# Performance work log

Hardware: AMD Instinct MI355X
Metric: run time of the kernel (lower is better)

Reference implementation:

```python
import jax, jax.numpy as jnp
import numpy as np

B, S, DIM = 4, 2048, 64
NUM_CODES = 65536
KCODES = 8


def setup_inputs() -> dict:
    key = jax.random.key(0)
    k1, k2 = jax.random.split(key)
    x = jax.random.normal(k1, (B, S, DIM), dtype=jnp.float32)
    codebook = jax.random.normal(k2, (NUM_CODES, DIM), dtype=jnp.float32)
    return {"x": x, "codebook": codebook}


def reference(x, codebook):
    """EuclideanSnapFunction.forward, keep_k_codes path with no disabled codes.

    logits = -cdist(x, codebook, p=2); topk(kcodes); embedding gather; mean.
    sqrt is monotonic, so top-k on negative *squared* distance yields identical
    indices (and identical outputs) while avoiding the sqrt.
    """
    x2 = jnp.sum(x * x, axis=-1, keepdims=True)          # [B,S,1]
    c2 = jnp.sum(codebook * codebook, axis=-1)           # [N]
    xc = jnp.einsum("bsd,nd->bsn", x, codebook)          # [B,S,N]
    neg_d2 = 2.0 * xc - x2 - c2                           # = -squared dist
    _, codebook_ids = jax.lax.top_k(neg_d2, KCODES)      # [B,S,K]
    codes = codebook[codebook_ids]                        # [B,S,K,D] gather
    outputs = codes.sum(axis=-2) / KCODES                 # [B,S,D]
    return outputs, codebook_ids
```

## Files before the change

### kernel.cpp

```cpp
#include <hip/hip_runtime.h>
#include <float.h>

#define DIM     64
#define NCODES  65536
#define KC      8
#define NQ      8192
#define KROW    80
#define CS      32
#define CHUNK   (NCODES/CS)
#define NITER   (CHUNK/32)
#define NVIEW   64
#define CAP     12
#define DELTA   1.5f
#define MAXSUR  384

typedef __bf16 bf16x8 __attribute__((ext_vector_type(8)));
typedef float  f32x16 __attribute__((ext_vector_type(16)));
typedef unsigned short u16x8 __attribute__((ext_vector_type(8)));

static __device__ __forceinline__ unsigned short f2bf(float f) {
    unsigned u = __float_as_uint(f);
    u += 0x7FFFu + ((u >> 16) & 1u);
    return (unsigned short)(u >> 16);
}

#define RJ(j) (((j) & 3) + 8 * ((j) >> 2))

__global__ __launch_bounds__(256) void k_conv_cb(const float* __restrict__ cb,
                                                 unsigned short* __restrict__ cbb) {
    int n = blockIdx.x * 256 + threadIdx.x;
    const float4* src = (const float4*)(cb + (size_t)n * DIM);
    unsigned short* dst = cbb + (size_t)n * KROW;
    float s = 0.f;
#pragma unroll
    for (int c = 0; c < 8; ++c) {
        float4 f0 = src[2 * c], f1 = src[2 * c + 1];
        s = fmaf(f0.x, f0.x, s); s = fmaf(f0.y, f0.y, s);
        s = fmaf(f0.z, f0.z, s); s = fmaf(f0.w, f0.w, s);
        s = fmaf(f1.x, f1.x, s); s = fmaf(f1.y, f1.y, s);
        s = fmaf(f1.z, f1.z, s); s = fmaf(f1.w, f1.w, s);
        u16x8 o;
        o[0] = f2bf(2.f * f0.x); o[1] = f2bf(2.f * f0.y);
        o[2] = f2bf(2.f * f0.z); o[3] = f2bf(2.f * f0.w);
        o[4] = f2bf(2.f * f1.x); o[5] = f2bf(2.f * f1.y);
        o[6] = f2bf(2.f * f1.z); o[7] = f2bf(2.f * f1.w);
        *(u16x8*)(dst + c * 8) = o;
    }
    unsigned short hi = f2bf(s);
    float hif = __uint_as_float(((unsigned)hi) << 16);
    unsigned short lo = f2bf(s - hif);
    u16x8 p = { (unsigned short)(hi ^ 0x8000u), (unsigned short)(lo ^ 0x8000u),
                0, 0, 0, 0, 0, 0 };
    *(u16x8*)(dst + 64) = p;
    u16x8 z = {0, 0, 0, 0, 0, 0, 0, 0};
    *(u16x8*)(dst + 72) = z;
}

__global__ __launch_bounds__(256) void k_conv_x(const float* __restrict__ x,
                                                unsigned short* __restrict__ xb) {
    int n = blockIdx.x * 256 + threadIdx.x;
    const float4* src = (const float4*)(x + (size_t)n * DIM);
    unsigned short* dst = xb + (size_t)n * KROW;
#pragma unroll
    for (int c = 0; c < 8; ++c) {
        float4 f0 = src[2 * c], f1 = src[2 * c + 1];
        u16x8 o;
        o[0] = f2bf(f0.x); o[1] = f2bf(f0.y); o[2] = f2bf(f0.z); o[3] = f2bf(f0.w);
        o[4] = f2bf(f1.x); o[5] = f2bf(f1.y); o[6] = f2bf(f1.z); o[7] = f2bf(f1.w);
        *(u16x8*)(dst + c * 8) = o;
    }
    u16x8 p = {0x3F80u, 0x3F80u, 0, 0, 0, 0, 0, 0};
    *(u16x8*)(dst + 64) = p;
    u16x8 z = {0, 0, 0, 0, 0, 0, 0, 0};
    *(u16x8*)(dst + 72) = z;
}

__device__ __forceinline__ float tmax16(const f32x16& a) {
    const float m0 = fmaxf(fmaxf(a[0],  a[1]),  a[2]);
    const float m1 = fmaxf(fmaxf(a[3],  a[4]),  a[5]);
    const float m2 = fmaxf(fmaxf(a[6],  a[7]),  a[8]);
    const float m3 = fmaxf(fmaxf(a[9],  a[10]), a[11]);
    const float m4 = fmaxf(fmaxf(a[12], a[13]), a[14]);
    const float n0 = fmaxf(fmaxf(m0, m1), m2);
    const float n1 = fmaxf(fmaxf(m3, m4), a[15]);
    return fmaxf(n0, n1);
}

__global__ __launch_bounds__(256, 4) void k_scanA(const unsigned short* __restrict__ cbb_,
                                                  const unsigned short* __restrict__ xb_,
                                                  float* __restrict__ top1) {
    const __bf16* cbv = (const __bf16*)cbb_;
    const __bf16* xbv = (const __bf16*)xb_;
    const int tid = threadIdx.x, lane = tid & 63, wv = tid >> 6;
    const int laneh = lane >> 5;
    const int qg = blockIdx.x >> 5;
    const int cs = blockIdx.x & 31;
    const int qA = qg * 256 + wv * 64 + (lane & 31);
    const int qB = qA + 32;
    const int cbase = cs * CHUNK;
    const int view = cs * 2 + laneh;

    bf16x8 bfrA[5], bfrB[5];
    {
        const __bf16* bp = xbv + (size_t)qA * KROW + laneh * 8;
#pragma unroll
        for (int s = 0; s < 5; ++s) bfrA[s] = *(const bf16x8*)(bp + s * 16);
        bp += (size_t)32 * KROW;
#pragma unroll
        for (int s = 0; s < 5; ++s) bfrB[s] = *(const bf16x8*)(bp + s * 16);
    }

    float t1a = -FLT_MAX, t1b = -FLT_MAX;

    const __bf16* ap = cbv + (size_t)(cbase + (lane & 31)) * KROW + laneh * 8;
    bf16x8 fA[5], fB[5];
#pragma unroll
    for (int s = 0; s < 5; ++s) fA[s] = *(const bf16x8*)(ap + s * 16);
#pragma unroll
    for (int s = 0; s < 5; ++s) fB[s] = *(const bf16x8*)(ap + 32 * KROW + s * 16);
    ap += 64 * KROW;

    for (int it = 0; it < NITER; it += 2) {
        {
            f32x16 acc = {0,0,0,0, 0,0,0,0, 0,0,0,0, 0,0,0,0};
#pragma unroll
            for (int s = 0; s < 5; ++s)
                acc = __builtin_amdgcn_mfma_f32_32x32x16_bf16(fA[s], bfrA[s], acc, 0, 0, 0);
            t1a = fmaxf(t1a, tmax16(acc));
            f32x16 acc2 = {0,0,0,0, 0,0,0,0, 0,0,0,0, 0,0,0,0};
#pragma unroll
            for (int s = 0; s < 5; ++s)
                acc2 = __builtin_amdgcn_mfma_f32_32x32x16_bf16(fA[s], bfrB[s], acc2, 0, 0, 0);
#pragma unroll
            for (int s = 0; s < 5; ++s) fA[s] = *(const bf16x8*)(ap + s * 16);
            t1b = fmaxf(t1b, tmax16(acc2));
        }
        {
            f32x16 acc = {0,0,0,0, 0,0,0,0, 0,0,0,0, 0,0,0,0};
#pragma unroll
            for (int s = 0; s < 5; ++s)
                acc = __builtin_amdgcn_mfma_f32_32x32x16_bf16(fB[s], bfrA[s], acc, 0, 0, 0);
            t1a = fmaxf(t1a, tmax16(acc));
            f32x16 acc2 = {0,0,0,0, 0,0,0,0, 0,0,0,0, 0,0,0,0};
#pragma unroll
            for (int s = 0; s < 5; ++s)
                acc2 = __builtin_amdgcn_mfma_f32_32x32x16_bf16(fB[s], bfrB[s], acc2, 0, 0, 0);
#pragma unroll
            for (int s = 0; s < 5; ++s) fB[s] = *(const bf16x8*)(ap + 32 * KROW + s * 16);
            t1b = fmaxf(t1b, tmax16(acc2));
        }
        ap += 64 * KROW;
    }

    top1[(size_t)qA * NVIEW + view] = t1a;
    top1[(size_t)qB * NVIEW + view] = t1b;
}

__global__ __launch_bounds__(256) void k_thresh(const float* __restrict__ top1,
                                                float* __restrict__ thrm) {
    const int lane = threadIdx.x & 63;
    const int q = blockIdx.x * 4 + (threadIdx.x >> 6);
    float v = top1[(size_t)q * NVIEW + lane];
    float mx = -FLT_MAX;
#pragma unroll
    for (int r = 0; r < 8; ++r) {
        mx = v;
#pragma unroll
        for (int off = 32; off; off >>= 1) mx = fmaxf(mx, __shfl_xor(mx, off, 64));
        if (v == mx) v = -FLT_MAX;
    }
    if (lane == 0) thrm[q] = mx - DELTA;
}

__global__ __launch_bounds__(256, 4) void k_collect(const unsigned short* __restrict__ cbb_,
                                                    const unsigned short* __restrict__ xb_,
                                                    const float* __restrict__ thrm,
                                                    unsigned short* __restrict__ cand,
                                                    unsigned short* __restrict__ cnt) {
    const __bf16* cbv = (const __bf16*)cbb_;
    const __bf16* xbv = (const __bf16*)xb_;
    const int tid = threadIdx.x, lane = tid & 63, wv = tid >> 6;
    const int laneh = lane >> 5;
    const int qg = blockIdx.x >> 5;
    const int cs = blockIdx.x & 31;
    const int qA = qg * 256 + wv * 64 + (lane & 31);
    const int qB = qA + 32;
    const int cbase = cs * CHUNK;
    const int view = cs * 2 + laneh;

    bf16x8 bfrA[5], bfrB[5];
    {
        const __bf16* bp = xbv + (size_t)qA * KROW + laneh * 8;
#pragma unroll
        for (int s = 0; s < 5; ++s) bfrA[s] = *(const bf16x8*)(bp + s * 16);
        bp += (size_t)32 * KROW;
#pragma unroll
        for (int s = 0; s < 5; ++s) bfrB[s] = *(const bf16x8*)(bp + s * 16);
    }
    const float TmA = thrm[qA];
    const float TmB = thrm[qB];
    unsigned cA = 0, cB = 0;
    unsigned short* bufA = cand + ((size_t)qA * NVIEW + view) * CAP;
    unsigned short* bufB = cand + ((size_t)qB * NVIEW + view) * CAP;

    const __bf16* ap = cbv + (size_t)(cbase + (lane & 31)) * KROW + laneh * 8;
    bf16x8 fA[5], fB[5];
#pragma unroll
    for (int s = 0; s < 5; ++s) fA[s] = *(const bf16x8*)(ap + s * 16);
#pragma unroll
    for (int s = 0; s < 5; ++s) fB[s] = *(const bf16x8*)(ap + 32 * KROW + s * 16);
    ap += 64 * KROW;

    for (int it = 0; it < NITER; it += 2) {
        {
            const int code0 = cbase + it * 32 + 4 * laneh;
            f32x16 acc = {0,0,0,0, 0,0,0,0, 0,0,0,0, 0,0,0,0};
#pragma unroll
            for (int s = 0; s < 5; ++s)
                acc = __builtin_amdgcn_mfma_f32_32x32x16_bf16(fA[s], bfrA[s], acc, 0, 0, 0);
            if (__any(tmax16(acc) >= TmA)) {
#pragma unroll
                for (int j = 0; j < 16; ++j)
                    if (acc[j] >= TmA) { if (cA < CAP) bufA[cA] = (unsigned short)(code0 + RJ(j)); ++cA; }
            }
            f32x16 acc2 = {0,0,0,0, 0,0,0,0, 0,0,0,0, 0,0,0,0};
#pragma unroll
            for (int s = 0; s < 5; ++s)
                acc2 = __builtin_amdgcn_mfma_f32_32x32x16_bf16(fA[s], bfrB[s], acc2, 0, 0, 0);
#pragma unroll
            for (int s = 0; s < 5; ++s) fA[s] = *(const bf16x8*)(ap + s * 16);
            if (__any(tmax16(acc2) >= TmB)) {
#pragma unroll
                for (int j = 0; j < 16; ++j)
                    if (acc2[j] >= TmB) { if (cB < CAP) bufB[cB] = (unsigned short)(code0 + RJ(j)); ++cB; }
            }
        }
        {
            const int code0 = cbase + (it + 1) * 32 + 4 * laneh;
            f32x16 acc = {0,0,0,0, 0,0,0,0, 0,0,0,0, 0,0,0,0};
#pragma unroll
            for (int s = 0; s < 5; ++s)
                acc = __builtin_amdgcn_mfma_f32_32x32x16_bf16(fB[s], bfrA[s], acc, 0, 0, 0);
            if (__any(tmax16(acc) >= TmA)) {
#pragma unroll
                for (int j = 0; j < 16; ++j)
                    if (acc[j] >= TmA) { if (cA < CAP) bufA[cA] = (unsigned short)(code0 + RJ(j)); ++cA; }
            }
            f32x16 acc2 = {0,0,0,0, 0,0,0,0, 0,0,0,0, 0,0,0,0};
#pragma unroll
            for (int s = 0; s < 5; ++s)
                acc2 = __builtin_amdgcn_mfma_f32_32x32x16_bf16(fB[s], bfrB[s], acc2, 0, 0, 0);
#pragma unroll
            for (int s = 0; s < 5; ++s) fB[s] = *(const bf16x8*)(ap + 32 * KROW + s * 16);
            if (__any(tmax16(acc2) >= TmB)) {
#pragma unroll
                for (int j = 0; j < 16; ++j)
                    if (acc2[j] >= TmB) { if (cB < CAP) bufB[cB] = (unsigned short)(code0 + RJ(j)); ++cB; }
            }
        }
        ap += 64 * KROW;
    }
    cnt[(size_t)qA * NVIEW + view] = (unsigned short)(cA < CAP ? cA : CAP);
    cnt[(size_t)qB * NVIEW + view] = (unsigned short)(cB < CAP ? cB : CAP);
}

__device__ __forceinline__ float np_pairwise_sq64(const float* __restrict__ p) {
    float r[8];
#pragma unroll
    for (int j = 0; j < 8; ++j) r[j] = __fmul_rn(p[j], p[j]);
#pragma unroll
    for (int k = 1; k < 8; ++k)
#pragma unroll
        for (int j = 0; j < 8; ++j)
            r[j] = __fadd_rn(r[j], __fmul_rn(p[8 * k + j], p[8 * k + j]));
    const float t01 = __fadd_rn(r[0], r[1]);
    const float t23 = __fadd_rn(r[2], r[3]);
    const float t45 = __fadd_rn(r[4], r[5]);
    const float t67 = __fadd_rn(r[6], r[7]);
    return __fadd_rn(__fadd_rn(t01, t23), __fadd_rn(t45, t67));
}

__device__ __forceinline__ float score_key(const float* __restrict__ xr,
                                           const float* __restrict__ cr,
                                           float x2e) {
    float xc = 0.f;
#pragma unroll
    for (int d = 0; d < DIM; ++d) xc = __builtin_fmaf(cr[d], xr[d], xc);
    const float c2e = np_pairwise_sq64(cr);
    return __fsub_rn(__fsub_rn(__fmul_rn(2.0f, xc), x2e), c2e);
}

__global__ __launch_bounds__(256) void k_rescore(const float* __restrict__ x,
                                                 const float* __restrict__ cb,
                                                 const unsigned short* __restrict__ cand,
                                                 const unsigned short* __restrict__ cnt,
                                                 float* __restrict__ out0,
                                                 float* __restrict__ out1) {
    __shared__ int s_ids[4][MAXSUR];
    const int lane = threadIdx.x & 63;
    const int wvi = threadIdx.x >> 6;
    const int q = blockIdx.x * 4 + wvi;
    const float* xr = x + ((size_t)q << 6);
    const float x2e = np_pairwise_sq64(xr);

    const int c = cnt[(size_t)q * NVIEW + lane];
    int p = c;
#pragma unroll
    for (int off = 1; off < 64; off <<= 1) {
        const int t = __shfl_up(p, off, 64);
        if (lane >= off) p += t;
    }
    const int excl = p - c;
    int total = __shfl(p, 63, 64);
    if (total > MAXSUR) total = MAXSUR;
    const unsigned short* src = cand + ((size_t)q * NVIEW + lane) * CAP;
    for (int k = 0; k < c; ++k) {
        const int dst = excl + k;
        if (dst < MAXSUR) s_ids[wvi][dst] = src[k];
    }
    __syncthreads();

    float vv[6]; int id[6];
#pragma unroll
    for (int s = 0; s < 6; ++s) {
        vv[s] = -FLT_MAX; id[s] = 1 << 20;
        if (s * 64 < total) {
            const int pos = lane + 64 * s;
            if (pos < total) {
                const int idv = s_ids[wvi][pos];
                id[s] = idv;
                vv[s] = score_key(xr, cb + (size_t)idv * DIM, x2e);
            }
        }
    }

    double accd = 0.0;
#pragma unroll
    for (int rep = 0; rep < KC; ++rep) {
        float bv = vv[0]; int bi = id[0];
#pragma unroll
        for (int s = 1; s < 6; ++s)
            if (vv[s] > bv || (vv[s] == bv && id[s] < bi)) { bv = vv[s]; bi = id[s]; }
#pragma unroll
        for (int off = 32; off; off >>= 1) {
            const float ov = __shfl_xor(bv, off, 64);
            const int   oi = __shfl_xor(bi, off, 64);
            if (ov > bv || (ov == bv && oi < bi)) { bv = ov; bi = oi; }
        }
        if (lane == 0) out1[q * KC + rep] = (float)bi;
        accd += (double)cb[(size_t)bi * DIM + lane];
#pragma unroll
        for (int s = 0; s < 6; ++s) if (id[s] == bi) vv[s] = -FLT_MAX;
    }
    out0[(size_t)q * DIM + lane] = (float)(accd * 0.125);
}

extern "C" void kernel_launch(void* const* d_in, const int* in_sizes, int n_in,
                              void* d_out, int out_size, void* d_ws, size_t ws_size,
                              hipStream_t stream) {
    const float* x  = (const float*)d_in[0];
    const float* cb = (const float*)d_in[1];

    char* ws = (char*)d_ws;
    unsigned short* cbb  = (unsigned short*)ws;
    unsigned short* xb   = (unsigned short*)(ws + (size_t)NCODES * KROW * 2);
    float*          top1 = (float*)(ws + (size_t)NCODES * KROW * 2
                                       + (size_t)NQ * KROW * 2);
    float*          thrm = (float*)((char*)top1 + (size_t)NQ * NVIEW * 4);
    unsigned short* cnt  = (unsigned short*)((char*)thrm + (size_t)NQ * 4);
    unsigned short* cand = (unsigned short*)((char*)cnt + (size_t)NQ * NVIEW * 2);

    float* out0 = (float*)d_out;
    float* out1 = (float*)d_out + (size_t)NQ * DIM;

    k_conv_cb<<<NCODES / 256, 256, 0, stream>>>(cb, cbb);
    k_conv_x <<<NQ / 256,     256, 0, stream>>>(x, xb);
    k_scanA  <<<1024,         256, 0, stream>>>(cbb, xb, top1);
    k_thresh <<<NQ / 4,       256, 0, stream>>>(top1, thrm);
    k_collect<<<1024,         256, 0, stream>>>(cbb, xb, thrm, cand, cnt);
    k_rescore<<<NQ / 4,       256, 0, stream>>>(x, cb, cand, cnt, out0, out1);
}
```

Baseline: 218.1 us.

## Stage codebook tiles through double-buffered LDS and split codebook into 64 chunks

The scan and collect kernels now cooperatively load 64-code codebook tiles into double-buffered shared memory and read MFMA operands from LDS, instead of each wave loading its own copy straight from global memory. Four waves in a block share one tile, which cuts redundant global and L2 traffic. The codebook split also goes from 32 to 64 chunks, so the grid doubles to 2048 blocks and there are 128 views per query with a per-view cap of 6. This adds a block barrier every iteration and changes the threshold and rescore indexing. Halving the per-view cap raises the risk of candidate truncation.

Result: slower. 224.8 us (+3.1%).

```diff
diff --git a/kernel.cpp b/kernel.cpp
--- a/kernel.cpp
+++ b/kernel.cpp
@@ -6,11 +6,15 @@
 #define KC      8
 #define NQ      8192
 #define KROW    80
-#define CS      32
+#define GPITCH  160
+#define LPITCH  176
+#define TILEG   5120
+#define TILEL   5632
+#define CS      64
 #define CHUNK   (NCODES/CS)
 #define NITER   (CHUNK/32)
-#define NVIEW   64
-#define CAP     12
+#define NVIEW   128
+#define CAP     6
 #define DELTA   1.5f
 #define MAXSUR  384
 
@@ -86,19 +90,31 @@
     return fmaxf(n0, n1);
 }
 
+__device__ __forceinline__ float4 stage_ld(const char* gt, int t, int r, int h) {
+    const int tile = (t >= 5) ? 1 : 0;
+    const int g16 = (h + 2 * (t - tile * 5)) * 16;
+    return *(const float4*)(gt + tile * TILEG + r * GPITCH + g16);
+}
+__device__ __forceinline__ void stage_st(unsigned char* lb, int t, int r, int h, float4 v) {
+    const int tile = (t >= 5) ? 1 : 0;
+    const int g16 = (h + 2 * (t - tile * 5)) * 16;
+    *(float4*)(lb + tile * TILEL + r * LPITCH + g16) = v;
+}
+
 __global__ __launch_bounds__(256, 4) void k_scanA(const unsigned short* __restrict__ cbb_,
                                                   const unsigned short* __restrict__ xb_,
                                                   float* __restrict__ top1) {
-    const __bf16* cbv = (const __bf16*)cbb_;
+    __shared__ __align__(16) unsigned char smem[2][2 * TILEL];
     const __bf16* xbv = (const __bf16*)xb_;
     const int tid = threadIdx.x, lane = tid & 63, wv = tid >> 6;
-    const int laneh = lane >> 5;
-    const int qg = blockIdx.x >> 5;
-    const int cs = blockIdx.x & 31;
-    const int qA = qg * 256 + wv * 64 + (lane & 31);
+    const int laneh = lane >> 5, lrow = lane & 31;
+    const int qg = blockIdx.x >> 6;
+    const int cs = blockIdx.x & 63;
+    const int qA = qg * 256 + wv * 64 + lrow;
     const int qB = qA + 32;
     const int cbase = cs * CHUNK;
     const int view = cs * 2 + laneh;
+    const char* cbbytes = (const char*)cbb_;
 
     bf16x8 bfrA[5], bfrB[5];
     {
@@ -110,46 +126,47 @@
         for (int s = 0; s < 5; ++s) bfrB[s] = *(const bf16x8*)(bp + s * 16);
     }
 
+    {
+        const char* gt = cbbytes + (size_t)cbase * GPITCH;
+        stage_st(smem[0], wv,     lrow, laneh, stage_ld(gt, wv,     lrow, laneh));
+        stage_st(smem[0], wv + 4, lrow, laneh, stage_ld(gt, wv + 4, lrow, laneh));
+        if (wv < 2)
+            stage_st(smem[0], wv + 8, lrow, laneh, stage_ld(gt, wv + 8, lrow, laneh));
+    }
+    __syncthreads();
+
     float t1a = -FLT_MAX, t1b = -FLT_MAX;
-
-    const __bf16* ap = cbv + (size_t)(cbase + (lane & 31)) * KROW + laneh * 8;
-    bf16x8 fA[5], fB[5];
-#pragma unroll
-    for (int s = 0; s < 5; ++s) fA[s] = *(const bf16x8*)(ap + s * 16);
-#pragma unroll
-    for (int s = 0; s < 5; ++s) fB[s] = *(const bf16x8*)(ap + 32 * KROW + s * 16);
-    ap += 64 * KROW;
+    int cur = 0;
 
     for (int it = 0; it < NITER; it += 2) {
-        {
-            f32x16 acc = {0,0,0,0, 0,0,0,0, 0,0,0,0, 0,0,0,0};
-#pragma unroll
-            for (int s = 0; s < 5; ++s)
-                acc = __builtin_amdgcn_mfma_f32_32x32x16_bf16(fA[s], bfrA[s], acc, 0, 0, 0);
+        const char* gt = cbbytes + (size_t)(cbase + (it + 2) * 32) * GPITCH;
+        float4 r0 = stage_ld(gt, wv,     lrow, laneh);
+        float4 r1 = stage_ld(gt, wv + 4, lrow, laneh);
+        float4 r2 = {0, 0, 0, 0};
+        if (wv < 2) r2 = stage_ld(gt, wv + 8, lrow, laneh);
+
+        const unsigned char* tb0 = smem[cur] + lrow * LPITCH + laneh * 16;
+#pragma unroll
+        for (int t = 0; t < 2; ++t) {
+            const unsigned char* tb = tb0 + t * TILEL;
+            f32x16 acc  = {0,0,0,0, 0,0,0,0, 0,0,0,0, 0,0,0,0};
+            f32x16 acc2 = {0,0,0,0, 0,0,0,0, 0,0,0,0, 0,0,0,0};
+#pragma unroll
+            for (int s = 0; s < 5; ++s) {
+                const bf16x8 a = *(const bf16x8*)(tb + s * 32);
+                acc  = __builtin_amdgcn_mfma_f32_32x32x16_bf16(a, bfrA[s], acc,  0, 0, 0);
+                acc2 = __builtin_amdgcn_mfma_f32_32x32x16_bf16(a, bfrB[s], acc2, 0, 0, 0);
+            }
             t1a = fmaxf(t1a, tmax16(acc));
-            f32x16 acc2 = {0,0,0,0, 0,0,0,0, 0,0,0,0, 0,0,0,0};
-#pragma unroll
-            for (int s = 0; s < 5; ++s)
-                acc2 = __builtin_amdgcn_mfma_f32_32x32x16_bf16(fA[s], bfrB[s], acc2, 0, 0, 0);
-#pragma unroll
-            for (int s = 0; s < 5; ++s) fA[s] = *(const bf16x8*)(ap + s * 16);
             t1b = fmaxf(t1b, tmax16(acc2));
         }
-        {
-            f32x16 acc = {0,0,0,0, 0,0,0,0, 0,0,0,0, 0,0,0,0};
-#pragma unroll
-            for (int s = 0; s < 5; ++s)
-                acc = __builtin_amdgcn_mfma_f32_32x32x16_bf16(fB[s], bfrA[s], acc, 0, 0, 0);
-            t1a = fmaxf(t1a, tmax16(acc));
-            f32x16 acc2 = {0,0,0,0, 0,0,0,0, 0,0,0,0, 0,0,0,0};
-#pragma unroll
-            for (int s = 0; s < 5; ++s)
-                acc2 = __builtin_amdgcn_mfma_f32_32x32x16_bf16(fB[s], bfrB[s], acc2, 0, 0, 0);
-#pragma unroll
-            for (int s = 0; s < 5; ++s) fB[s] = *(const bf16x8*)(ap + 32 * KROW + s * 16);
-            t1b = fmaxf(t1b, tmax16(acc2));
-        }
-        ap += 64 * KROW;
+
+        unsigned char* nb = smem[cur ^ 1];
+        stage_st(nb, wv,     lrow, laneh, r0);
+        stage_st(nb, wv + 4, lrow, laneh, r1);
+        if (wv < 2) stage_st(nb, wv + 8, lrow, laneh, r2);
+        __syncthreads();
+        cur ^= 1;
     }
 
     top1[(size_t)qA * NVIEW + view] = t1a;
@@ -160,14 +177,16 @@
                                                 float* __restrict__ thrm) {
     const int lane = threadIdx.x & 63;
     const int q = blockIdx.x * 4 + (threadIdx.x >> 6);
-    float v = top1[(size_t)q * NVIEW + lane];
+    float2 t = *(const float2*)(top1 + (size_t)q * NVIEW + lane * 2);
+    float v0 = t.x, v1 = t.y;
     float mx = -FLT_MAX;
 #pragma unroll
     for (int r = 0; r < 8; ++r) {
-        mx = v;
+        mx = fmaxf(v0, v1);
 #pragma unroll
         for (int off = 32; off; off >>= 1) mx = fmaxf(mx, __shfl_xor(mx, off, 64));
-        if (v == mx) v = -FLT_MAX;
+        if (v0 == mx) v0 = -FLT_MAX;
+        if (v1 == mx) v1 = -FLT_MAX;
     }
     if (lane == 0) thrm[q] = mx - DELTA;
 }
@@ -177,16 +196,17 @@
                                                     const float* __restrict__ thrm,
                                                     unsigned short* __restrict__ cand,
                                                     unsigned short* __restrict__ cnt) {
-    const __bf16* cbv = (const __bf16*)cbb_;
+    __shared__ __align__(16) unsigned char smem[2][2 * TILEL];
     const __bf16* xbv = (const __bf16*)xb_;
     const int tid = threadIdx.x, lane = tid & 63, wv = tid >> 6;
-    const int laneh = lane >> 5;
-    const int qg = blockIdx.x >> 5;
-    const int cs = blockIdx.x & 31;
-    const int qA = qg * 256 + wv * 64 + (lane & 31);
+    const int laneh = lane >> 5, lrow = lane & 31;
+    const int qg = blockIdx.x >> 6;
+    const int cs = blockIdx.x & 63;
+    const int qA = qg * 256 + wv * 64 + lrow;
     const int qB = qA + 32;
     const int cbase = cs * CHUNK;
     const int view = cs * 2 + laneh;
+    const char* cbbytes = (const char*)cbb_;
 
     bf16x8 bfrA[5], bfrB[5];
     {
@@ -203,62 +223,54 @@
     unsigned short* bufA = cand + ((size_t)qA * NVIEW + view) * CAP;
     unsigned short* bufB = cand + ((size_t)qB * NVIEW + view) * CAP;
 
-    const __bf16* ap = cbv + (size_t)(cbase + (lane & 31)) * KROW + laneh * 8;
-    bf16x8 fA[5], fB[5];
-#pragma unroll
-    for (int s = 0; s < 5; ++s) fA[s] = *(const bf16x8*)(ap + s * 16);
-#pragma unroll
-    for (int s = 0; s < 5; ++s) fB[s] = *(const bf16x8*)(ap + 32 * KROW + s * 16);
-    ap += 64 * KROW;
-
+    {
+        const char* gt = cbbytes + (size_t)cbase * GPITCH;
+        stage_st(smem[0], wv,     lrow, laneh, stage_ld(gt, wv,     lrow, laneh));
+        stage_st(smem[0], wv + 4, lrow, laneh, stage_ld(gt, wv + 4, lrow, laneh));
+        if (wv < 2)
+            stage_st(smem[0], wv + 8, lrow, laneh, stage_ld(gt, wv + 8, lrow, laneh));
+    }
+    __syncthreads();
+
+    int cur = 0;
     for (int it = 0; it < NITER; it += 2) {
-        {
-            const int code0 = cbase + it * 32 + 4 * laneh;
-            f32x16 acc = {0,0,0,0, 0,0,0,0, 0,0,0,0, 0,0,0,0};
-#pragma unroll
-            for (int s = 0; s < 5; ++s)
-                acc = __builtin_amdgcn_mfma_f32_32x32x16_bf16(fA[s], bfrA[s], acc, 0, 0, 0);
+        const char* gt = cbbytes + (size_t)(cbase + (it + 2) * 32) * GPITCH;
+        float4 r0 = stage_ld(gt, wv,     lrow, laneh);
+        float4 r1 = stage_ld(gt, wv + 4, lrow, laneh);
+        float4 r2 = {0, 0, 0, 0};
+        if (wv < 2) r2 = stage_ld(gt, wv + 8, lrow, laneh);
+
+        const unsigned char* tb0 = smem[cur] + lrow * LPITCH + laneh * 16;
+#pragma unroll
+        for (int t = 0; t < 2; ++t) {
+            const unsigned char* tb = tb0 + t * TILEL;
+            f32x16 acc  = {0,0,0,0, 0,0,0,0, 0,0,0,0, 0,0,0,0};
+            f32x16 acc2 = {0,0,0,0, 0,0,0,0, 0,0,0,0, 0,0,0,0};
+#pragma unroll
+            for (int s = 0; s < 5; ++s) {
+                const bf16x8 a = *(const bf16x8*)(tb + s * 32);
+                acc  = __builtin_amdgcn_mfma_f32_32x32x16_bf16(a, bfrA[s], acc,  0, 0, 0);
+                acc2 = __builtin_amdgcn_mfma_f32_32x32x16_bf16(a, bfrB[s], acc2, 0, 0, 0);
+            }
+            const int code0 = cbase + (it + t) * 32 + 4 * laneh;
             if (__any(tmax16(acc) >= TmA)) {
 #pragma unroll
                 for (int j = 0; j < 16; ++j)
                     if (acc[j] >= TmA) { if (cA < CAP) bufA[cA] = (unsigned short)(code0 + RJ(j)); ++cA; }
             }
-            f32x16 acc2 = {0,0,0,0, 0,0,0,0, 0,0,0,0, 0,0,0,0};
-#pragma unroll
-            for (int s = 0; s < 5; ++s)
-                acc2 = __builtin_amdgcn_mfma_f32_32x32x16_bf16(fA[s], bfrB[s], acc2, 0, 0, 0);
-#pragma unroll
-            for (int s = 0; s < 5; ++s) fA[s] = *(const bf16x8*)(ap + s * 16);
             if (__any(tmax16(acc2) >= TmB)) {
 #pragma unroll
                 for (int j = 0; j < 16; ++j)
                     if (acc2[j] >= TmB) { if (cB < CAP) bufB[cB] = (unsigned short)(code0 + RJ(j)); ++cB; }
             }
         }
-        {
-            const int code0 = cbase + (it + 1) * 32 + 4 * laneh;
-            f32x16 acc = {0,0,0,0, 0,0,0,0, 0,0,0,0, 0,0,0,0};
-#pragma unroll
-            for (int s = 0; s < 5; ++s)
-                acc = __builtin_amdgcn_mfma_f32_32x32x16_bf16(fB[s], bfrA[s], acc, 0, 0, 0);
-            if (__any(tmax16(acc) >= TmA)) {
-#pragma unroll
-                for (int j = 0; j < 16; ++j)
-                    if (acc[j] >= TmA) { if (cA < CAP) bufA[cA] = (unsigned short)(code0 + RJ(j)); ++cA; }
-            }
-            f32x16 acc2 = {0,0,0,0, 0,0,0,0, 0,0,0,0, 0,0,0,0};
-#pragma unroll
-            for (int s = 0; s < 5; ++s)
-                acc2 = __builtin_amdgcn_mfma_f32_32x32x16_bf16(fB[s], bfrB[s], acc2, 0, 0, 0);
-#pragma unroll
-            for (int s = 0; s < 5; ++s) fB[s] = *(const bf16x8*)(ap + 32 * KROW + s * 16);
-            if (__any(tmax16(acc2) >= TmB)) {
-#pragma unroll
-                for (int j = 0; j < 16; ++j)
-                    if (acc2[j] >= TmB) { if (cB < CAP) bufB[cB] = (unsigned short)(code0 + RJ(j)); ++cB; }
-            }
-        }
-        ap += 64 * KROW;
+
+        unsigned char* nb = smem[cur ^ 1];
+        stage_st(nb, wv,     lrow, laneh, r0);
+        stage_st(nb, wv + 4, lrow, laneh, r1);
+        if (wv < 2) stage_st(nb, wv + 8, lrow, laneh, r2);
+        __syncthreads();
+        cur ^= 1;
     }
     cnt[(size_t)qA * NVIEW + view] = (unsigned short)(cA < CAP ? cA : CAP);
     cnt[(size_t)qB * NVIEW + view] = (unsigned short)(cB < CAP ? cB : CAP);
@@ -303,7 +315,9 @@
     const float* xr = x + ((size_t)q << 6);
     const float x2e = np_pairwise_sq64(xr);
 
-    const int c = cnt[(size_t)q * NVIEW + lane];
+    const int c0 = cnt[(size_t)q * NVIEW + 2 * lane];
+    const int c1 = cnt[(size_t)q * NVIEW + 2 * lane + 1];
+    const int c = c0 + c1;
     int p = c;
 #pragma unroll
     for (int off = 1; off < 64; off <<= 1) {
@@ -313,10 +327,15 @@
     const int excl = p - c;
     int total = __shfl(p, 63, 64);
     if (total > MAXSUR) total = MAXSUR;
-    const unsigned short* src = cand + ((size_t)q * NVIEW + lane) * CAP;
-    for (int k = 0; k < c; ++k) {
+    const unsigned short* s0 = cand + ((size_t)q * NVIEW + 2 * lane) * CAP;
+    for (int k = 0; k < c0; ++k) {
         const int dst = excl + k;
-        if (dst < MAXSUR) s_ids[wvi][dst] = src[k];
+        if (dst < MAXSUR) s_ids[wvi][dst] = s0[k];
+    }
+    const unsigned short* s1 = s0 + CAP;
+    for (int k = 0; k < c1; ++k) {
+        const int dst = excl + c0 + k;
+        if (dst < MAXSUR) s_ids[wvi][dst] = s1[k];
     }
     __syncthreads();
 
@@ -375,8 +394,8 @@
 
     k_conv_cb<<<NCODES / 256, 256, 0, stream>>>(cb, cbb);
     k_conv_x <<<NQ / 256,     256, 0, stream>>>(x, xb);
-    k_scanA  <<<1024,         256, 0, stream>>>(cbb, xb, top1);
+    k_scanA  <<<2048,         256, 0, stream>>>(cbb, xb, top1);
     k_thresh <<<NQ / 4,       256, 0, stream>>>(top1, thrm);
-    k_collect<<<1024,         256, 0, stream>>>(cbb, xb, thrm, cand, cnt);
+    k_collect<<<2048,         256, 0, stream>>>(cbb, xb, thrm, cand, cnt);
     k_rescore<<<NQ / 4,       256, 0, stream>>>(x, cb, cand, cnt, out0, out1);
 }
```
